# Optimization experiments

Hardware: AMD Instinct MI355X
Metric: run time of the kernel (lower is better)

## Reference

```python
import jax, jax.numpy as jnp
import numpy as np

NEIGHBOUR = 3  # matches init_kwargs['neighbour']


def _conv2d(x, w, b=None, stride=1, pad=0):
    out = jax.lax.conv_general_dilated(
        x, w, (stride, stride), [(pad, pad), (pad, pad)],
        dimension_numbers=('NCHW', 'OIHW', 'NCHW'))
    if b is not None:
        out = out + b[None, :, None, None]
    return out


def _warp(x, offset, wg_w, wg_b, conv_w):
    """Deformable bilinear warp: offsets -> 4 corner gathers -> modulate -> regroup -> strided conv."""
    k = NEIGHBOUR
    N = k * k
    B, C, H, W = x.shape
    m = jax.nn.sigmoid(_conv2d(x, wg_w, wg_b, 1, 1))          # [B,N,H,W] modulation gate
    xp = jnp.pad(x, ((0, 0), (0, 0), (1, 1), (1, 1)))         # zero pad -> [B,C,H+2,W+2]
    Hp, Wp = H + 2, W + 2
    r = jnp.arange(-(k - 1) // 2, (k - 1) // 2 + 1, dtype=x.dtype)
    pnx, pny = jnp.meshgrid(r, r, indexing='ij')              # kernel-neighbour offsets p_n
    # absolute sampling positions in padded coords (p_0 starts at 1 due to padding)
    p0x = jnp.arange(1, H + 1, dtype=x.dtype)[None, :, None, None]
    p0y = jnp.arange(1, W + 1, dtype=x.dtype)[None, None, :, None]
    off = offset.transpose(0, 2, 3, 1)                        # [B,H,W,2N]; first N = x, last N = y
    px = p0x + pnx.ravel()[None, None, None, :] + off[..., :N]  # [B,H,W,N]
    py = p0y + pny.ravel()[None, None, None, :] + off[..., N:]
    fx = jnp.floor(jax.lax.stop_gradient(px))                 # p.detach().floor()
    fy = jnp.floor(jax.lax.stop_gradient(py))
    qx_lt = jnp.clip(fx, 0, Hp - 1)
    qy_lt = jnp.clip(fy, 0, Wp - 1)
    qx_rb = jnp.clip(fx + 1, 0, Hp - 1)
    qy_rb = jnp.clip(fy + 1, 0, Wp - 1)
    px = jnp.clip(px, 0, Hp - 1)
    py = jnp.clip(py, 0, Wp - 1)
    # bilinear weights (same algebra as the torch code)
    g_lt = (1 + (qx_lt - px)) * (1 + (qy_lt - py))
    g_rb = (1 - (qx_rb - px)) * (1 - (qy_rb - py))
    g_lb = (1 + (qx_lt - px)) * (1 - (qy_rb - py))
    g_rt = (1 - (qx_rb - px)) * (1 + (qy_lt - py))
    ix_lt = qx_lt.astype(jnp.int32); iy_lt = qy_lt.astype(jnp.int32)
    ix_rb = qx_rb.astype(jnp.int32); iy_rb = qy_rb.astype(jnp.int32)
    x_flat = xp.reshape(B, C, Hp * Wp)

    def gather(ix, iy):
        idx = (ix * Wp + iy).reshape(B, 1, H * W * N)
        return jnp.take_along_axis(x_flat, idx, axis=-1).reshape(B, C, H, W, N)

    xw = (g_lt[:, None] * gather(ix_lt, iy_lt)
          + g_rb[:, None] * gather(ix_rb, iy_rb)
          + g_lb[:, None] * gather(ix_lt, iy_rb)
          + g_rt[:, None] * gather(ix_rb, iy_lt))              # [B,C,H,W,N]
    xw = xw * m.transpose(0, 2, 3, 1)[:, None]                 # modulation, broadcast over C
    # regroup [B,C,H,W,k,k] -> [B,C,H*k,W*k] (matches _reshape_x_warped ordering)
    xw = xw.reshape(B, C, H, W, k, k).transpose(0, 1, 2, 4, 3, 5).reshape(B, C, H * k, W * k)
    return _conv2d(xw, conv_w, None, stride=k, pad=0)          # grouped-back strided conv


def setup_inputs() -> dict:
    B, C, MH, H, W = 4, 64, 18, 128, 128  # MH = 2*neighbour^2
    key = jax.random.key(0)
    ks = jax.random.split(key, 12)
    f32 = jnp.float32
    s = 0.05  # weight scale to keep gates unsaturated
    return {
        'x_t': jax.random.normal(ks[0], (B, C, H, W), f32),
        'pre_offset': jax.random.normal(ks[1], (B, MH, H, W), f32),
        'mean': jax.random.normal(ks[2], (B, MH, H, W), f32),
        'upd_w': s * jax.random.normal(ks[3], (MH, C + MH, 3, 3), f32),
        'upd_b': s * jax.random.normal(ks[4], (MH,), f32),
        'rst_w': s * jax.random.normal(ks[5], (MH, C + MH, 3, 3), f32),
        'rst_b': s * jax.random.normal(ks[6], (MH,), f32),
        'out_w': s * jax.random.normal(ks[7], (MH, C + MH, 3, 3), f32),
        'out_b': s * jax.random.normal(ks[8], (MH,), f32),
        'wg_w': s * jax.random.normal(ks[9], (9, C, 3, 3), f32),
        'wg_b': s * jax.random.normal(ks[10], (9,), f32),
        'warp_conv_w': s * jax.random.normal(ks[11], (C, C, 3, 3), f32),
    }


def reference(x_t, pre_offset, mean, upd_w, upd_b, rst_w, rst_b, out_w, out_b,
              wg_w, wg_b, warp_conv_w):
    stacked = jnp.concatenate([x_t, pre_offset], axis=1)
    update_gate = jax.nn.sigmoid(_conv2d(stacked, upd_w, upd_b, 1, 1))
    reset_gate = jax.nn.sigmoid(_conv2d(stacked, rst_w, rst_b, 1, 1))
    cand = jnp.tanh(_conv2d(jnp.concatenate([x_t, pre_offset * reset_gate], axis=1), out_w, out_b, 1, 1))
    offset = pre_offset * (1 - update_gate) + cand * update_gate
    mean_new = mean + 0.5 * (pre_offset - mean)
    offset = offset + mean_new
    x_out = _warp(x_t, offset, wg_w, wg_b, warp_conv_w)
    return (x_out, offset, mean_new)
```

## Files before the change

### kernel.cpp

```cpp
#include <hip/hip_runtime.h>
#include <hip/hip_bf16.h>
#include <math.h>

#define Bn  4
#define Cc  64
#define MHc 18
#define Hh  128
#define Wd  128
#define HW  (Hh*Wd)
#define Np  9
#define HP  130
#define WP  130
#define XPE (HP*WP*Cc)
#define PPE (HP*WP*32)
#define KX  576
#define KP  288
#define KT  (KX+KP)

typedef __attribute__((ext_vector_type(8))) short short8;
typedef __attribute__((ext_vector_type(4))) float float4v;

__device__ __forceinline__ float bf2f(__hip_bfloat16 x) { return __bfloat162float(x); }
__device__ __forceinline__ __hip_bfloat16 f2bf(float x) { return __float2bfloat16(x); }
__device__ __forceinline__ float sigm(float x) { return 1.f / (1.f + expf(-x)); }
__device__ __forceinline__ float s2f(short s) {
  return __uint_as_float(((unsigned)(unsigned short)s) << 16);
}
__device__ __forceinline__ short f2bs(float x) {
  __hip_bfloat16 h = __float2bfloat16(x);
  return *reinterpret_cast<short*>(&h);
}

#define NW1 (64*KT)
#define NW2 (32*KP)
#define NW3 (Cc*Cc*Np)

__global__ __launch_bounds__(256)
void k_prep(const float* __restrict__ x, const float* __restrict__ po,
            const float* __restrict__ upd_w, const float* __restrict__ rst_w,
            const float* __restrict__ out_w, const float* __restrict__ wg_w,
            const float* __restrict__ wcw,
            __hip_bfloat16* __restrict__ xp, __hip_bfloat16* __restrict__ pp,
            __hip_bfloat16* __restrict__ wall, __hip_bfloat16* __restrict__ w2,
            __hip_bfloat16* __restrict__ wt) {
  __shared__ float tile[128][65];
  int blk = blockIdx.x;
  int t = threadIdx.x;
  if (blk < 512) {
    int b = blk >> 7, h = blk & 127;
    int c = t >> 2;
    int wbase = (t & 3) * 32;
    const float* src = &x[(b*Cc + c)*HW + h*Wd + wbase];
    #pragma unroll
    for (int j = 0; j < 8; ++j) {
      float4v v = *reinterpret_cast<const float4v*>(src + j*4);
      tile[wbase + j*4 + 0][c] = v.x;
      tile[wbase + j*4 + 1][c] = v.y;
      tile[wbase + j*4 + 2][c] = v.z;
      tile[wbase + j*4 + 3][c] = v.w;
    }
    __syncthreads();
    #pragma unroll
    for (int j = 0; j < 4; ++j) {
      int i = t + j * 256;
      int px = i >> 3, oct = i & 7;
      short8 ov;
      #pragma unroll
      for (int e = 0; e < 8; ++e) ov[e] = f2bs(tile[px][oct*8 + e]);
      *reinterpret_cast<short8*>(
          &xp[b*XPE + ((h+1)*WP + px + 1)*Cc + oct*8]) = ov;
    }
  } else if (blk < 1024) {
    int pb = blk - 512;
    int h = pb & 127;
    int b = pb >> 7;
    int w = t & 127;
    int half = t >> 7;
    float v[9];
    #pragma unroll
    for (int j = 0; j < 9; ++j)
      v[j] = po[(b*MHc + half*9 + j)*HW + h*Wd + w];
    #pragma unroll
    for (int j = 0; j < 9; ++j)
      pp[b*PPE + ((h+1)*WP + (w+1))*32 + half*9 + j] = f2bf(v[j]);
  } else {
    int idx = (blk - 1024) * 256 + t;
    if (idx < NW1) {
      int k  = idx % KT;
      int gr = idx / KT;
      float v = 0.f;
      if (k < KX) {
        int n = k >> 6, ci = k & 63;
        if      (gr < 18) v = upd_w[(gr*(Cc+MHc) + ci)*9 + n];
        else if (gr < 36) v = rst_w[((gr-18)*(Cc+MHc) + ci)*9 + n];
        else if (gr < 54) v = out_w[((gr-36)*(Cc+MHc) + ci)*9 + n];
        else if (gr < 63) v = wg_w[((gr-54)*Cc + ci)*9 + n];
      } else {
        int kk = k - KX;
        int n = kk >> 5, jc = kk & 31;
        if (jc < 18) {
          if      (gr < 18) v = upd_w[(gr*(Cc+MHc) + Cc + jc)*9 + n];
          else if (gr < 36) v = rst_w[((gr-18)*(Cc+MHc) + Cc + jc)*9 + n];
        }
      }
      wall[idx] = f2bf(v);
    } else if (idx < NW1 + NW2) {
      int i2 = idx - NW1;
      int k  = i2 % KP;
      int oc = i2 / KP;
      int n = k >> 5, jc = k & 31;
      float v = (oc < 18 && jc < 18) ? out_w[(oc*(Cc+MHc) + Cc + jc)*9 + n] : 0.f;
      w2[i2] = f2bf(v);
    } else if (idx < NW1 + NW2 + NW3) {
      int i3 = idx - NW1 - NW2;
      int k  = i3 % 576;
      int co = i3 / 576;
      wt[i3] = f2bf(wcw[(co*Cc + (k & 63))*9 + (k >> 6)]);
    }
  }
}

__global__ __launch_bounds__(256)
void k_gates(const __hip_bfloat16* __restrict__ xpad,
             const __hip_bfloat16* __restrict__ popad,
             const __hip_bfloat16* __restrict__ wall,
             const float* __restrict__ po,
             const float* __restrict__ upd_b,
             const float* __restrict__ rst_b,
             const float* __restrict__ out_b,
             const float* __restrict__ wg_b,
             float* __restrict__ u_out,
             float* __restrict__ cx_out,
             __hip_bfloat16* __restrict__ ropad,
             __hip_bfloat16* __restrict__ m_t) {
  __shared__ __align__(16) char winx[13056];
  __shared__ __align__(16) char winp[6528];
  __shared__ __align__(16) __hip_bfloat16 roL[32][32];
  int blk = blockIdx.x;
  int wtile = blk & 3;
  int h = (blk >> 2) & 127;
  int b = blk >> 9;
  int w0 = wtile * 32;
  int lane = threadIdx.x & 63;
  int wave = threadIdx.x >> 6;
  int t = threadIdx.x;

  ((unsigned int*)roL)[t] = 0u;
  ((unsigned int*)roL)[t + 256] = 0u;

  const __hip_bfloat16* xpb = xpad + b * XPE;
  const __hip_bfloat16* ppb = popad + b * PPE;

  for (int i = t; i < 816; i += 256) {
    int r = i / 272, cidx = i - r * 272;
    short8 v = *reinterpret_cast<const short8*>(
        xpb + ((h + r) * WP + w0) * Cc + cidx * 8);
    int o = i * 16;
    *reinterpret_cast<short8*>(winx + (o ^ (((o >> 7) & 7) << 4))) = v;
  }
  for (int i = t; i < 408; i += 256) {
    int r = i / 136, cidx = i - r * 136;
    short8 v = *reinterpret_cast<const short8*>(
        ppb + ((h + r) * WP + w0) * 32 + cidx * 8);
    int o = i * 16;
    *reinterpret_cast<short8*>(winp + (o ^ (((o >> 6) & 3) << 4))) = v;
  }
  __syncthreads();

  int mrow = lane & 15;
  int quad = lane >> 4;
  int cotile = wave * 16;
  float4v acc0 = {0.f, 0.f, 0.f, 0.f};
  float4v acc1 = {0.f, 0.f, 0.f, 0.f};
  #pragma unroll
  for (int ks = 0; ks < KT/32; ++ks) {
    short8 a = *reinterpret_cast<const short8*>(
        wall + (cotile + mrow) * KT + ks * 32 + quad * 8);
    short8 b0, b1;
    if (ks < 18) {
      int n = ks >> 1;
      int r0i = (n / 3) * 34 + mrow + (n % 3);
      int r1i = r0i + 16;
      int l0 = r0i * 128 + (ks & 1) * 64 + quad * 16;
      int l1 = r1i * 128 + (ks & 1) * 64 + quad * 16;
      b0 = *reinterpret_cast<const short8*>(winx + (l0 ^ ((r0i & 7) << 4)));
      b1 = *reinterpret_cast<const short8*>(winx + (l1 ^ ((r1i & 7) << 4)));
    } else {
      int n = ks - 18;
      int r0i = (n / 3) * 34 + mrow + (n % 3);
      int r1i = r0i + 16;
      int l0 = r0i * 64 + quad * 16;
      int l1 = r1i * 64 + quad * 16;
      b0 = *reinterpret_cast<const short8*>(winp + (l0 ^ ((r0i & 3) << 4)));
      b1 = *reinterpret_cast<const short8*>(winp + (l1 ^ ((r1i & 3) << 4)));
    }
    acc0 = __builtin_amdgcn_mfma_f32_16x16x32_bf16(a, b0, acc0, 0, 0, 0);
    acc1 = __builtin_amdgcn_mfma_f32_16x16x32_bf16(a, b1, acc1, 0, 0, 0);
  }

  int sp0 = h * Wd + w0 + mrow;
  int sp1 = sp0 + 16;
  float pv0[4], pv1[4];
  #pragma unroll
  for (int r = 0; r < 4; ++r) {
    int gr = cotile + quad * 4 + r;
    if (gr >= 18 && gr < 36) {
      pv0[r] = po[(b*MHc + (gr-18))*HW + sp0];
      pv1[r] = po[(b*MHc + (gr-18))*HW + sp1];
    }
  }
  #pragma unroll
  for (int r = 0; r < 4; ++r) {
    int gr = cotile + quad * 4 + r;
    float v0 = acc0[r], v1 = acc1[r];
    if (gr < 18) {
      u_out[(b*MHc + gr)*HW + sp0] = sigm(v0 + upd_b[gr]);
      u_out[(b*MHc + gr)*HW + sp1] = sigm(v1 + upd_b[gr]);
    } else if (gr < 36) {
      int oc = gr - 18;
      roL[mrow][oc]      = f2bf(sigm(v0 + rst_b[oc]) * pv0[r]);
      roL[16 + mrow][oc] = f2bf(sigm(v1 + rst_b[oc]) * pv1[r]);
    } else if (gr < 54) {
      int oc = gr - 36;
      cx_out[(b*MHc + oc)*HW + sp0] = v0 + out_b[oc];
      cx_out[(b*MHc + oc)*HW + sp1] = v1 + out_b[oc];
    } else if (gr < 63) {
      int nn = gr - 54;
      m_t[nn*(Bn*HW) + b*HW + sp0] = f2bf(sigm(v0 + wg_b[nn]));
      m_t[nn*(Bn*HW) + b*HW + sp1] = f2bf(sigm(v1 + wg_b[nn]));
    }
  }
  __syncthreads();
  unsigned int* dst = (unsigned int*)(ropad + b*PPE + ((h+1)*WP + (w0+1))*32);
  dst[t] = ((unsigned int*)roL)[t];
  dst[t + 256] = ((unsigned int*)roL)[t + 256];
}

__global__ __launch_bounds__(256)
void k_fuse(const __hip_bfloat16* __restrict__ xpad,
            const __hip_bfloat16* __restrict__ ropad,
            const __hip_bfloat16* __restrict__ w2,
            const __hip_bfloat16* __restrict__ wt,
            const __hip_bfloat16* __restrict__ m_t,
            const float* __restrict__ po,
            const float* __restrict__ mean,
            float* __restrict__ out_off,
            float* __restrict__ out_mn,
            float* __restrict__ out_x) {
  __shared__ __align__(16) char lbuf[16*584*2];
  __shared__ float offL[16][18];
  __shared__ float mL[16][9];
  __shared__ __align__(16) float gw[144][4];
  __shared__ __align__(16) int   ga[144][2];
  auto xw = (__hip_bfloat16(*)[584])lbuf;

  int blk = blockIdx.x;
  int wtile = blk & 7;
  int h = (blk >> 3) & 127;
  int b = blk >> 10;
  int w0 = wtile * 16;
  int lane = threadIdx.x & 63;
  int wave = threadIdx.x >> 6;
  int t = threadIdx.x;

  int mrow = lane & 15;
  int quad = lane >> 4;

  float ov[4], uv[4], pv[4], mv[4];
  int gil[4];
  if (wave < 2) {
    int sp = h * Wd + w0 + mrow;
    #pragma unroll
    for (int r = 0; r < 4; ++r) {
      int gr = wave*16 + quad * 4 + r;
      gil[r] = (b*MHc + gr)*HW + sp;
      if (gr < 18) {
        ov[r] = out_off[gil[r]];
        uv[r] = out_mn[gil[r]];
        pv[r] = po[gil[r]];
        mv[r] = mean[gil[r]];
      }
    }
  }

  const __hip_bfloat16* rpb = ropad + b * PPE;
  if (t < 216) {
    int r = t / 72, cidx = t - r * 72;
    short8 v = *reinterpret_cast<const short8*>(
        rpb + ((h + r) * WP + w0) * 32 + cidx * 8);
    int o = t * 16;
    *reinterpret_cast<short8*>(lbuf + (o ^ (((o >> 6) & 3) << 4))) = v;
  }
  if (t < 144) {
    int n = t >> 4, px = t & 15;
    mL[px][n] = bf2f(m_t[n*(Bn*HW) + b*HW + h*Wd + w0 + px]);
  }
  __syncthreads();

  if (wave < 2) {
    float4v acc = {0.f, 0.f, 0.f, 0.f};
    #pragma unroll
    for (int ks = 0; ks < KP/32; ++ks) {
      short8 a = *reinterpret_cast<const short8*>(
          w2 + (wave*16 + mrow) * KP + ks * 32 + quad * 8);
      int rowidx = (ks / 3) * 18 + mrow + (ks % 3);
      int lin = rowidx * 64 + quad * 16;
      short8 bfr = *reinterpret_cast<const short8*>(
          lbuf + (lin ^ ((rowidx & 3) << 4)));
      acc = __builtin_amdgcn_mfma_f32_16x16x32_bf16(a, bfr, acc, 0, 0, 0);
    }
    #pragma unroll
    for (int r = 0; r < 4; ++r) {
      int gr = wave*16 + quad * 4 + r;
      if (gr < 18) {
        float cand = tanhf(ov[r] + acc[r]);
        float mn = 0.5f * (mv[r] + pv[r]);
        float off = pv[r] * (1.f - uv[r]) + cand * uv[r] + mn;
        out_off[gil[r]] = off;
        out_mn[gil[r]]  = mn;
        offL[mrow][gr] = off;
      }
    }
  }
  __syncthreads();

  if (t < 144) {
    int px = t / 9;
    int n = t - px * 9;
    int wp = w0 + px;
    float ox = offL[px][n];
    float oy = offL[px][9 + n];
    float mnv = mL[px][n];
    float px_ = (float)(h + 1) + (float)(n / 3 - 1) + ox;
    float py_ = (float)(wp + 1) + (float)(n % 3 - 1) + oy;
    float fx = floorf(px_), fy = floorf(py_);
    float xlt = fminf(fmaxf(fx,       0.f), 129.f);
    float ylt = fminf(fmaxf(fy,       0.f), 129.f);
    float xrb = fminf(fmaxf(fx + 1.f, 0.f), 129.f);
    float yrb = fminf(fmaxf(fy + 1.f, 0.f), 129.f);
    float pxc = fminf(fmaxf(px_, 0.f), 129.f);
    float pyc = fminf(fmaxf(py_, 0.f), 129.f);
    float glt = (1.f + xlt - pxc) * (1.f + ylt - pyc);
    float grb = (1.f - xrb + pxc) * (1.f - yrb + pyc);
    float glb = (1.f + xlt - pxc) * (1.f - yrb + pyc);
    float grt = (1.f - xrb + pxc) * (1.f + ylt - pyc);
    int ixl = (int)xlt, iyl = (int)ylt, ixr = (int)xrb, iyr = (int)yrb;
    bool yAdj = (iyr == iyl + 1);
    gw[t][0] = (glt + (yAdj ? 0.f : glb)) * mnv;
    gw[t][1] = (yAdj ? glb : 0.f) * mnv;
    gw[t][2] = (grt + (yAdj ? 0.f : grb)) * mnv;
    gw[t][3] = (yAdj ? grb : 0.f) * mnv;
    ga[t][0] = (ixl * WP + iyl) * Cc;
    ga[t][1] = (ixr * WP + iyl) * Cc;
  }
  __syncthreads();

  const __hip_bfloat16* xpb = xpad + b * XPE;
  for (int it = t; it < 1152; it += 256) {
    int q  = it >> 3;
    int c0 = (it & 7) * 8;
    float4v g = *reinterpret_cast<const float4v*>(gw[q]);
    int bL = ga[q][0] + c0, bR = ga[q][1] + c0;
    short8 l0 = *reinterpret_cast<const short8*>(xpb + bL);
    short8 l1 = *reinterpret_cast<const short8*>(xpb + bL + 64);
    short8 r0 = *reinterpret_cast<const short8*>(xpb + bR);
    short8 r1 = *reinterpret_cast<const short8*>(xpb + bR + 64);
    short8 ovv;
    #pragma unroll
    for (int j = 0; j < 8; ++j) {
      float vv = g.x * s2f(l0[j]);
      vv = fmaf(g.y, s2f(l1[j]), vv);
      vv = fmaf(g.z, s2f(r0[j]), vv);
      vv = fmaf(g.w, s2f(r1[j]), vv);
      ovv[j] = f2bs(vv);
    }
    int pl = q / 9;
    int n  = q - pl * 9;
    *reinterpret_cast<short8*>(&xw[pl][n * 64 + c0]) = ovv;
  }
  __syncthreads();

  int cotile = wave * 16;
  float4v acc = {0.f, 0.f, 0.f, 0.f};
  for (int ks = 0; ks < 18; ++ks) {
    short8 a = *reinterpret_cast<const short8*>(
        wt + (cotile + mrow) * 576 + ks * 32 + quad * 8);
    short8 bfr = *reinterpret_cast<const short8*>(
        &xw[mrow][ks * 32 + quad * 8]);
    acc = __builtin_amdgcn_mfma_f32_16x16x32_bf16(a, bfr, acc, 0, 0, 0);
  }
  #pragma unroll
  for (int r = 0; r < 4; ++r) {
    int co = cotile + quad * 4 + r;
    out_x[((b * Cc + co) * Hh + h) * Wd + w0 + mrow] = acc[r];
  }
}

__global__ void f_convAB(const float* __restrict__ x, const float* __restrict__ po,
                         const float* __restrict__ wA, const float* __restrict__ bA,
                         const float* __restrict__ wB, const float* __restrict__ bB,
                         float* __restrict__ u_scr, float* __restrict__ ro_scr) {
  int idx = blockIdx.x * 256 + threadIdx.x;
  if (idx >= Bn * MHc * HW) return;
  int w = idx & 127, h = (idx >> 7) & 127, oc = (idx >> 14) % MHc, b = idx / (MHc*HW);
  float accA = bA[oc], accB = bB[oc];
  const float* xb = x + b*Cc*HW; const float* pb = po + b*MHc*HW;
  for (int ic = 0; ic < Cc + MHc; ++ic) {
    const float* src = (ic < Cc) ? (xb + ic*HW) : (pb + (ic-Cc)*HW);
    const float* wa = wA + (oc*(Cc+MHc)+ic)*9; const float* wb = wB + (oc*(Cc+MHc)+ic)*9;
    for (int kh = 0; kh < 3; ++kh) { int hh = h+kh-1; if ((unsigned)hh >= Hh) continue;
      for (int kw = 0; kw < 3; ++kw) { int ww = w+kw-1; if ((unsigned)ww >= Wd) continue;
        float v = src[hh*Wd+ww]; accA += v*wa[kh*3+kw]; accB += v*wb[kh*3+kw]; } }
  }
  u_scr[idx] = sigm(accA); ro_scr[idx] = sigm(accB) * pb[oc*HW + h*Wd + w];
}
__global__ void f_convC(const float* __restrict__ x, const float* __restrict__ po,
                        const float* __restrict__ mean, const float* __restrict__ wC,
                        const float* __restrict__ bC, const float* __restrict__ u_scr,
                        const float* __restrict__ ro_scr, float* __restrict__ out_off,
                        float* __restrict__ out_mean) {
  int idx = blockIdx.x * 256 + threadIdx.x;
  if (idx >= Bn * MHc * HW) return;
  int w = idx & 127, h = (idx >> 7) & 127, oc = (idx >> 14) % MHc, b = idx / (MHc*HW);
  float acc = bC[oc];
  const float* xb = x + b*Cc*HW; const float* rb = ro_scr + b*MHc*HW;
  for (int ic = 0; ic < Cc + MHc; ++ic) {
    const float* src = (ic < Cc) ? (xb + ic*HW) : (rb + (ic-Cc)*HW);
    const float* wv = wC + (oc*(Cc+MHc)+ic)*9;
    for (int kh = 0; kh < 3; ++kh) { int hh = h+kh-1; if ((unsigned)hh >= Hh) continue;
      for (int kw = 0; kw < 3; ++kw) { int ww = w+kw-1; if ((unsigned)ww >= Wd) continue;
        acc += src[hh*Wd+ww]*wv[kh*3+kw]; } }
  }
  float cand = tanhf(acc); float u = u_scr[idx]; float p = po[idx];
  float mn = 0.5f*(mean[idx]+p);
  out_off[idx] = p*(1.f-u)+cand*u+mn; out_mean[idx] = mn;
}
__global__ __launch_bounds__(256)
void f_warp(const float* __restrict__ x, const float* __restrict__ off_f,
            const float* __restrict__ wg, const float* __restrict__ bg,
            const float* __restrict__ wc, float* __restrict__ out) {
  __shared__ float mred[4][Np][64]; __shared__ float mval[4][Np];
  __shared__ float xwv[4][Np][64];
  int lane = threadIdx.x & 63, wave = threadIdx.x >> 6;
  int p = blockIdx.x * 4 + wave;
  int b = p >> 14, rem = p & 16383, h = rem >> 7, w = rem & 127;
  const float* xc = x + (b*Cc + lane)*HW;
  float part[Np];
  for (int n = 0; n < Np; ++n) part[n] = 0.f;
  for (int kh = 0; kh < 3; ++kh) { int hh = h+kh-1; if ((unsigned)hh >= Hh) continue;
    for (int kw = 0; kw < 3; ++kw) { int ww = w+kw-1; if ((unsigned)ww >= Wd) continue;
      float v = xc[hh*Wd+ww];
      for (int n = 0; n < Np; ++n) part[n] += v*wg[(n*Cc+lane)*9+kh*3+kw]; } }
  for (int n = 0; n < Np; ++n) mred[wave][n][lane] = part[n];
  __syncthreads();
  if (lane < Np) { float s = bg[lane];
    for (int c = 0; c < Cc; ++c) s += mred[wave][lane][c];
    mval[wave][lane] = sigm(s); }
  __syncthreads();
  const float* offb = off_f + b*MHc*HW; int sp = h*Wd + w;
  for (int n = 0; n < Np; ++n) {
    float px = (float)(h+1) + (float)(n/3-1) + offb[n*HW+sp];
    float py = (float)(w+1) + (float)(n%3-1) + offb[(9+n)*HW+sp];
    float fxq = floorf(px), fyq = floorf(py);
    float xlt = fminf(fmaxf(fxq,0.f),129.f), ylt = fminf(fmaxf(fyq,0.f),129.f);
    float xrb = fminf(fmaxf(fxq+1.f,0.f),129.f), yrb = fminf(fmaxf(fyq+1.f,0.f),129.f);
    float pxc = fminf(fmaxf(px,0.f),129.f), pyc = fminf(fmaxf(py,0.f),129.f);
    float glt = (1.f+xlt-pxc)*(1.f+ylt-pyc), grb = (1.f-xrb+pxc)*(1.f-yrb+pyc);
    float glb = (1.f+xlt-pxc)*(1.f-yrb+pyc), grt = (1.f-xrb+pxc)*(1.f+ylt-pyc);
    int ixl=(int)xlt, iyl=(int)ylt, ixr=(int)xrb, iyr=(int)yrb;
    float vlt=0.f,vrb=0.f,vlb=0.f,vrt=0.f;
    if (ixl>=1&&ixl<=Hh&&iyl>=1&&iyl<=Wd) vlt = xc[(ixl-1)*Wd+(iyl-1)];
    if (ixr>=1&&ixr<=Hh&&iyr>=1&&iyr<=Wd) vrb = xc[(ixr-1)*Wd+(iyr-1)];
    if (ixl>=1&&ixl<=Hh&&iyr>=1&&iyr<=Wd) vlb = xc[(ixl-1)*Wd+(iyr-1)];
    if (ixr>=1&&ixr<=Hh&&iyl>=1&&iyl<=Wd) vrt = xc[(ixr-1)*Wd+(iyl-1)];
    xwv[wave][n][lane] = (glt*vlt+grb*vrb+glb*vlb+grt*vrt)*mval[wave][n];
  }
  __syncthreads();
  float acc = 0.f;
  for (int c = 0; c < Cc; ++c)
    for (int n = 0; n < Np; ++n)
      acc += xwv[wave][n][c]*wc[(lane*Cc+c)*9+n];
  out[(b*Cc+lane)*HW + h*Wd + w] = acc;
}

extern "C" void kernel_launch(void* const* d_in, const int* in_sizes, int n_in,
                              void* d_out, int out_size, void* d_ws, size_t ws_size,
                              hipStream_t stream) {
  (void)in_sizes; (void)n_in; (void)out_size;
  const float* x_t   = (const float*)d_in[0];
  const float* po    = (const float*)d_in[1];
  const float* mean  = (const float*)d_in[2];
  const float* upd_w = (const float*)d_in[3];
  const float* upd_b = (const float*)d_in[4];
  const float* rst_w = (const float*)d_in[5];
  const float* rst_b = (const float*)d_in[6];
  const float* out_w = (const float*)d_in[7];
  const float* out_b = (const float*)d_in[8];
  const float* wg_w  = (const float*)d_in[9];
  const float* wg_b  = (const float*)d_in[10];
  const float* wcw   = (const float*)d_in[11];

  float* out_x   = (float*)d_out;
  float* out_off = out_x + 4194304;
  float* out_mn  = out_off + 1179648;

  char* ws = (char*)d_ws;
  __hip_bfloat16* xpad  = (__hip_bfloat16*)(ws + 0);
  __hip_bfloat16* popad = (__hip_bfloat16*)(ws + 8652800);
  __hip_bfloat16* ropad = (__hip_bfloat16*)(ws + 12979200);
  __hip_bfloat16* wall  = (__hip_bfloat16*)(ws + 17305600);
  __hip_bfloat16* w2    = (__hip_bfloat16*)(ws + 17416192);
  __hip_bfloat16* wt_bf = (__hip_bfloat16*)(ws + 17434624);
  __hip_bfloat16* m_t   = (__hip_bfloat16*)(ws + 17508352);
  const size_t WS_NEED = 18688000;

  if (ws_size >= WS_NEED) {
    hipMemsetAsync(d_ws, 0, 17305600, stream);
    hipLaunchKernelGGL(k_prep,  dim3(1420), dim3(256), 0, stream,
                       x_t, po, upd_w, rst_w, out_w, wg_w, wcw,
                       xpad, popad, wall, w2, wt_bf);
    hipLaunchKernelGGL(k_gates, dim3(2048), dim3(256), 0, stream,
                       xpad, popad, wall, po, upd_b, rst_b, out_b, wg_b,
                       out_mn, out_off, ropad, m_t);
    hipLaunchKernelGGL(k_fuse,  dim3(4096), dim3(256), 0, stream,
                       xpad, ropad, w2, wt_bf, m_t, po, mean,
                       out_off, out_mn, out_x);
  } else {
    float* u_scr  = out_x;
    float* cx_scr = out_x + 1179648;
    hipLaunchKernelGGL(f_convAB, dim3(4608), dim3(256), 0, stream,
                       x_t, po, upd_w, upd_b, rst_w, rst_b, u_scr, cx_scr);
    hipLaunchKernelGGL(f_convC,  dim3(4608), dim3(256), 0, stream,
                       x_t, po, mean, out_w, out_b, u_scr, cx_scr,
                       out_off, out_mn);
    hipLaunchKernelGGL(f_warp,   dim3(16384), dim3(256), 0, stream,
                       x_t, out_off, wg_w, wg_b, wcw, out_x);
  }
}
```

Baseline: 183.8 us.

## Zero only padding borders in prep kernel and double k_fuse pixel tile

The full-workspace memset is replaced by 12 extra k_prep blocks that zero only the one-pixel border of the padded x, pre-offset and reset-gate buffers, since the interiors are overwritten anyway. k_fuse now processes 32 pixels per block with 512 threads instead of 16 with 256, so the w2 and wt weight fragments are reused across two pixel groups and the reset-window rows shared between them are loaded once. Shared memory per block roughly doubles and launch bounds request 6 blocks, which may change occupancy. Relying on borders alone being zero assumes no other padding or slack regions are read.

```diff
diff --git a/kernel.cpp b/kernel.cpp
--- a/kernel.cpp
+++ b/kernel.cpp
@@ -41,6 +41,7 @@
             const float* __restrict__ out_w, const float* __restrict__ wg_w,
             const float* __restrict__ wcw,
             __hip_bfloat16* __restrict__ xp, __hip_bfloat16* __restrict__ pp,
+            __hip_bfloat16* __restrict__ rp,
             __hip_bfloat16* __restrict__ wall, __hip_bfloat16* __restrict__ w2,
             __hip_bfloat16* __restrict__ wt) {
   __shared__ float tile[128][65];
@@ -83,7 +84,7 @@
     #pragma unroll
     for (int j = 0; j < 9; ++j)
       pp[b*PPE + ((h+1)*WP + (w+1))*32 + half*9 + j] = f2bf(v[j]);
-  } else {
+  } else if (blk < 1420) {
     int idx = (blk - 1024) * 256 + t;
     if (idx < NW1) {
       int k  = idx % KT;
@@ -117,6 +118,46 @@
       int co = i3 / 576;
       wt[i3] = f2bf(wcw[(co*Cc + (k & 63))*9 + (k >> 6)]);
     }
+  } else {
+    int bid = blk - 1420;
+    int kind = bid >> 2;
+    int b = bid & 3;
+    short8 z = {0,0,0,0,0,0,0,0};
+    if (kind == 0) {
+      __hip_bfloat16* base = xp + b*XPE;
+      for (int i = t; i < 4128; i += 256) {
+        int off;
+        if (i < 2080) {
+          int row = (i < 1040) ? 0 : 129;
+          int j = (i < 1040) ? i : i - 1040;
+          off = row*130*64 + j*8;
+        } else {
+          int i2 = i - 2080;
+          int strip = i2 >> 3;
+          int r = 1 + (strip & 127);
+          int side = strip >> 7;
+          off = (r*130 + side*129)*64 + (i2 & 7)*8;
+        }
+        *reinterpret_cast<short8*>(base + off) = z;
+      }
+    } else {
+      __hip_bfloat16* base = (kind == 1 ? pp : rp) + b*PPE;
+      for (int i = t; i < 2064; i += 256) {
+        int off;
+        if (i < 1040) {
+          int row = (i < 520) ? 0 : 129;
+          int j = (i < 520) ? i : i - 520;
+          off = row*130*32 + j*8;
+        } else {
+          int i2 = i - 1040;
+          int strip = i2 >> 2;
+          int r = 1 + (strip & 127);
+          int side = strip >> 7;
+          off = (r*130 + side*129)*32 + (i2 & 3)*8;
+        }
+        *reinterpret_cast<short8*>(base + off) = z;
+      }
+    }
   }
 }
 
@@ -236,7 +277,7 @@
   dst[t + 256] = ((unsigned int*)roL)[t + 256];
 }
 
-__global__ __launch_bounds__(256)
+__global__ __launch_bounds__(512, 6)
 void k_fuse(const __hip_bfloat16* __restrict__ xpad,
             const __hip_bfloat16* __restrict__ ropad,
             const __hip_bfloat16* __restrict__ w2,
@@ -247,32 +288,32 @@
             float* __restrict__ out_off,
             float* __restrict__ out_mn,
             float* __restrict__ out_x) {
-  __shared__ __align__(16) char lbuf[16*584*2];
-  __shared__ float offL[16][18];
-  __shared__ float mL[16][9];
-  __shared__ __align__(16) float gw[144][4];
-  __shared__ __align__(16) int   ga[144][2];
+  __shared__ __align__(16) char lbuf[32*584*2];
+  __shared__ float offL[32][18];
+  __shared__ float mL[32][9];
+  __shared__ __align__(16) float gw[288][4];
+  __shared__ __align__(16) int   ga[288][2];
   auto xw = (__hip_bfloat16(*)[584])lbuf;
 
   int blk = blockIdx.x;
-  int wtile = blk & 7;
-  int h = (blk >> 3) & 127;
-  int b = blk >> 10;
-  int w0 = wtile * 16;
+  int wtile = blk & 3;
+  int h = (blk >> 2) & 127;
+  int b = blk >> 9;
+  int w0 = wtile * 32;
   int lane = threadIdx.x & 63;
-  int wave = threadIdx.x >> 6;
+  int wv = threadIdx.x >> 6;
   int t = threadIdx.x;
-
   int mrow = lane & 15;
   int quad = lane >> 4;
 
   float ov[4], uv[4], pv[4], mv[4];
   int gil[4];
-  if (wave < 2) {
-    int sp = h * Wd + w0 + mrow;
+  int am = wv & 1, pg = wv >> 1;
+  if (wv < 4) {
+    int sp = h * Wd + w0 + pg*16 + mrow;
     #pragma unroll
     for (int r = 0; r < 4; ++r) {
-      int gr = wave*16 + quad * 4 + r;
+      int gr = am*16 + quad * 4 + r;
       gil[r] = (b*MHc + gr)*HW + sp;
       if (gr < 18) {
         ov[r] = out_off[gil[r]];
@@ -284,26 +325,26 @@
   }
 
   const __hip_bfloat16* rpb = ropad + b * PPE;
-  if (t < 216) {
-    int r = t / 72, cidx = t - r * 72;
+  if (t < 408) {
+    int r = t / 136, cidx = t - r * 136;
     short8 v = *reinterpret_cast<const short8*>(
         rpb + ((h + r) * WP + w0) * 32 + cidx * 8);
     int o = t * 16;
     *reinterpret_cast<short8*>(lbuf + (o ^ (((o >> 6) & 3) << 4))) = v;
   }
-  if (t < 144) {
-    int n = t >> 4, px = t & 15;
+  if (t < 288) {
+    int n = t >> 5, px = t & 31;
     mL[px][n] = bf2f(m_t[n*(Bn*HW) + b*HW + h*Wd + w0 + px]);
   }
   __syncthreads();
 
-  if (wave < 2) {
+  if (wv < 4) {
     float4v acc = {0.f, 0.f, 0.f, 0.f};
     #pragma unroll
-    for (int ks = 0; ks < KP/32; ++ks) {
+    for (int ks = 0; ks < 9; ++ks) {
       short8 a = *reinterpret_cast<const short8*>(
-          w2 + (wave*16 + mrow) * KP + ks * 32 + quad * 8);
-      int rowidx = (ks / 3) * 18 + mrow + (ks % 3);
+          w2 + (am*16 + mrow) * KP + ks * 32 + quad * 8);
+      int rowidx = (ks / 3) * 34 + pg*16 + mrow + (ks % 3);
       int lin = rowidx * 64 + quad * 16;
       short8 bfr = *reinterpret_cast<const short8*>(
           lbuf + (lin ^ ((rowidx & 3) << 4)));
@@ -311,20 +352,20 @@
     }
     #pragma unroll
     for (int r = 0; r < 4; ++r) {
-      int gr = wave*16 + quad * 4 + r;
+      int gr = am*16 + quad * 4 + r;
       if (gr < 18) {
         float cand = tanhf(ov[r] + acc[r]);
         float mn = 0.5f * (mv[r] + pv[r]);
         float off = pv[r] * (1.f - uv[r]) + cand * uv[r] + mn;
         out_off[gil[r]] = off;
         out_mn[gil[r]]  = mn;
-        offL[mrow][gr] = off;
+        offL[pg*16 + mrow][gr] = off;
       }
     }
   }
   __syncthreads();
 
-  if (t < 144) {
+  if (t < 288) {
     int px = t / 9;
     int n = t - px * 9;
     int wp = w0 + px;
@@ -356,7 +397,7 @@
   __syncthreads();
 
   const __hip_bfloat16* xpb = xpad + b * XPE;
-  for (int it = t; it < 1152; it += 256) {
+  for (int it = t; it < 2304; it += 512) {
     int q  = it >> 3;
     int c0 = (it & 7) * 8;
     float4v g = *reinterpret_cast<const float4v*>(gw[q]);
@@ -380,19 +421,19 @@
   }
   __syncthreads();
 
-  int cotile = wave * 16;
+  int ct = wv & 3, pg5 = wv >> 2;
   float4v acc = {0.f, 0.f, 0.f, 0.f};
   for (int ks = 0; ks < 18; ++ks) {
     short8 a = *reinterpret_cast<const short8*>(
-        wt + (cotile + mrow) * 576 + ks * 32 + quad * 8);
+        wt + (ct*16 + mrow) * 576 + ks * 32 + quad * 8);
     short8 bfr = *reinterpret_cast<const short8*>(
-        &xw[mrow][ks * 32 + quad * 8]);
+        &xw[pg5*16 + mrow][ks * 32 + quad * 8]);
     acc = __builtin_amdgcn_mfma_f32_16x16x32_bf16(a, bfr, acc, 0, 0, 0);
   }
   #pragma unroll
   for (int r = 0; r < 4; ++r) {
-    int co = cotile + quad * 4 + r;
-    out_x[((b * Cc + co) * Hh + h) * Wd + w0 + mrow] = acc[r];
+    int co = ct*16 + quad * 4 + r;
+    out_x[((b * Cc + co) * Hh + h) * Wd + w0 + pg5*16 + mrow] = acc[r];
   }
 }
 
@@ -515,14 +556,13 @@
   const size_t WS_NEED = 18688000;
 
   if (ws_size >= WS_NEED) {
-    hipMemsetAsync(d_ws, 0, 17305600, stream);
-    hipLaunchKernelGGL(k_prep,  dim3(1420), dim3(256), 0, stream,
+    hipLaunchKernelGGL(k_prep,  dim3(1432), dim3(256), 0, stream,
                        x_t, po, upd_w, rst_w, out_w, wg_w, wcw,
-                       xpad, popad, wall, w2, wt_bf);
+                       xpad, popad, ropad, wall, w2, wt_bf);
     hipLaunchKernelGGL(k_gates, dim3(2048), dim3(256), 0, stream,
                        xpad, popad, wall, po, upd_b, rst_b, out_b, wg_b,
                        out_mn, out_off, ropad, m_t);
-    hipLaunchKernelGGL(k_fuse,  dim3(4096), dim3(256), 0, stream,
+    hipLaunchKernelGGL(k_fuse,  dim3(2048), dim3(512), 0, stream,
                        xpad, ropad, w2, wt_bf, m_t, po, mean,
                        out_off, out_mn, out_x);
   } else {
```

New measurement: 178.0 us. 1.03x faster.
